# Kernel tuning notes

Hardware: AMD Instinct MI355X
Metric: run time of the kernel (lower is better)

## Reference

```python
import jax, jax.numpy as jnp
import numpy as np

EPS = 1e-8  # torch cosine_similarity clamps norms at 1e-8
TEMPERATURE = 0.05


def _normalize(x):
    n = jnp.linalg.norm(x, axis=-1, keepdims=True)
    return x / jnp.maximum(n, EPS)


def setup_inputs() -> dict:
    key = jax.random.key(0)
    k1, k2, k3 = jax.random.split(key, 3)
    N, D = 8192, 256
    return {
        "text_embeddings": jax.random.normal(k1, (N, D), dtype=jnp.float32),
        "text_pos_embeddings": jax.random.normal(k2, (N, D), dtype=jnp.float32),
        "text_neg_embeddings": jax.random.normal(k3, (N, D), dtype=jnp.float32),
    }


def _pair_loss(a, b):
    # PairInBatchNegCoSentLoss(a, b): cos-sim matrix, scale, diag-subtract, LSE
    sim = _normalize(a) @ _normalize(b).T / TEMPERATURE  # [N, N]
    diff = sim - jnp.diagonal(sim)[:, None]
    return jax.nn.logsumexp(diff, axis=1).mean()


def reference(text_embeddings, text_pos_embeddings, text_neg_embeddings):
    e = _normalize(text_embeddings)
    p = _normalize(text_pos_embeddings)
    n = _normalize(text_neg_embeddings)
    sim_pos = jnp.sum(e * p, axis=-1)          # [N]
    sim_neg = e @ n.T                          # [N, N]
    sim = jnp.concatenate([sim_pos[:, None], sim_neg], axis=1) / TEMPERATURE
    diff = sim - sim[:, 0:1]
    loss = jax.nn.logsumexp(diff, axis=1).mean()
    # add_swap_loss=True: pair loss with (pos, anchor) swapped
    loss = loss + _pair_loss(text_pos_embeddings, text_embeddings)
    return loss
```

## Files before the change

kernel.cpp:

```cpp
#include <hip/hip_runtime.h>
#include <stdint.h>

#define N 8192
#define D 256
#define INV_T 20.0f
#define LOG2E 1.44269504088896340736f
#define BM 128
#define BN 128
#define NXB 64

typedef __attribute__((ext_vector_type(16))) float f32x16;
typedef __attribute__((ext_vector_type(4))) int i32x4;
typedef __attribute__((ext_vector_type(8))) int i32x8;

typedef __attribute__((address_space(3))) uint32_t lds_u32;
typedef __attribute__((address_space(1))) const uint32_t gbl_u32;

static __device__ __forceinline__ float fast_exp2(float x) {
#if __has_builtin(__builtin_amdgcn_exp2f)
  return __builtin_amdgcn_exp2f(x);
#else
  float r;
  asm("v_exp_f32 %0, %1" : "=v"(r) : "v"(x));
  return r;
#endif
}

#define DPP_ADD(v, ctrl)                                                      \
  ((v) + __builtin_bit_cast(float, __builtin_amdgcn_update_dpp(               \
             0, __builtin_bit_cast(int, (v)), (ctrl), 0xf, 0xf, true)))

__global__ __launch_bounds__(256) void normalize_kernel(
    const float* __restrict__ e, const float* __restrict__ p, const float* __restrict__ n,
    uint32_t* __restrict__ eb, uint32_t* __restrict__ pb, uint32_t* __restrict__ nb,
    float* __restrict__ cbuf) {
  const int tid = threadIdx.x;
  const int wave = tid >> 6, lane = tid & 63;
  const int row = blockIdx.x * 4 + wave;

  const float4 ev = ((const float4*)(e + (size_t)row * D))[lane];
  const float4 pv = ((const float4*)(p + (size_t)row * D))[lane];
  const float4 nv = ((const float4*)(n + (size_t)row * D))[lane];

  float sse = ev.x*ev.x + ev.y*ev.y + ev.z*ev.z + ev.w*ev.w;
  float ssp = pv.x*pv.x + pv.y*pv.y + pv.z*pv.z + pv.w*pv.w;
  float ssn = nv.x*nv.x + nv.y*nv.y + nv.z*nv.z + nv.w*nv.w;
  float dep = ev.x*pv.x + ev.y*pv.y + ev.z*pv.z + ev.w*pv.w;
#pragma unroll
  for (int m = 1; m < 64; m <<= 1) {
    sse += __shfl_xor(sse, m);
    ssp += __shfl_xor(ssp, m);
    ssn += __shfl_xor(ssn, m);
    dep += __shfl_xor(dep, m);
  }
  const float se = 1.0f / fmaxf(sqrtf(sse), 1e-8f);
  const float sp = 1.0f / fmaxf(sqrtf(ssp), 1e-8f);
  const float sn = 1.0f / fmaxf(sqrtf(ssn), 1e-8f);

  int ue = __builtin_amdgcn_cvt_pk_fp8_f32(ev.x*se, ev.y*se, 0, false);
  ue     = __builtin_amdgcn_cvt_pk_fp8_f32(ev.z*se, ev.w*se, ue, true);
  int up = __builtin_amdgcn_cvt_pk_fp8_f32(pv.x*sp, pv.y*sp, 0, false);
  up     = __builtin_amdgcn_cvt_pk_fp8_f32(pv.z*sp, pv.w*sp, up, true);
  int un = __builtin_amdgcn_cvt_pk_fp8_f32(nv.x*sn, nv.y*sn, 0, false);
  un     = __builtin_amdgcn_cvt_pk_fp8_f32(nv.z*sn, nv.w*sn, un, true);
  eb[row * 64 + lane] = (uint32_t)ue;
  pb[row * 64 + lane] = (uint32_t)up;
  nb[row * 64 + lane] = (uint32_t)un;

  if (lane == 0) cbuf[row] = dep * se * sp * INV_T;
}

__global__ __launch_bounds__(256, 3) void simexp_kernel(
    const uint8_t* __restrict__ eb, const uint8_t* __restrict__ pb,
    const uint8_t* __restrict__ nb, const float* __restrict__ cbuf,
    float* __restrict__ part) {
  __shared__ uint8_t Bs[BN * D];
  __shared__ float cs[BM];

  const int z = blockIdx.z;
  const uint8_t* __restrict__ A = z ? pb : eb;
  const uint8_t* __restrict__ B = z ? eb : nb;

  const int tid = threadIdx.x;
  const int wave = tid >> 6, lane = tid & 63;
  const int lane31 = lane & 31, half = lane >> 5;
  const int rowTile = blockIdx.x * BM, colblk = blockIdx.y;
  const int colTile = colblk * BN;

#pragma unroll
  for (int i = 0; i < 8; ++i) {
    const int c = i * 256 + tid, r = c >> 4, sl = c & 15;
    const int gg = sl ^ (r & 15);
    __builtin_amdgcn_global_load_lds(
        (gbl_u32*)(B + (size_t)(colTile + r) * D + gg * 16),
        (lds_u32*)&Bs[c * 16], 16, 0, 0);
  }

  const int arow = rowTile + wave * 32 + lane31;
  const uint8_t* __restrict__ Arow = A + (size_t)arow * D + half * 32;
  i32x8 afr[4];
#pragma unroll
  for (int s = 0; s < 4; ++s) {
    const i32x4 lo = *(const i32x4*)(Arow + s * 64);
    const i32x4 hi = *(const i32x4*)(Arow + s * 64 + 16);
    afr[s] = (i32x8){lo[0], lo[1], lo[2], lo[3], hi[0], hi[1], hi[2], hi[3]};
  }

  if (tid < BM) cs[tid] = cbuf[rowTile + tid] * LOG2E;

  int bbase[4];
#pragma unroll
  for (int ni = 0; ni < 4; ++ni) {
    const int cl = ni * 32 + lane31;
    bbase[ni] = (cl << 8) ^ ((cl & 15) << 4) ^ (half << 5);
  }

  f32x16 acc[4];
#pragma unroll
  for (int ni = 0; ni < 4; ++ni)
#pragma unroll
    for (int r = 0; r < 16; ++r) acc[ni][r] = 0.0f;

  __syncthreads();

#pragma unroll
  for (int s = 0; s < 4; ++s) {
#pragma unroll
    for (int ni = 0; ni < 4; ++ni) {
      const int alo = bbase[ni] ^ (s << 6);
      const i32x4 blo = *(const i32x4*)&Bs[alo];
      const i32x4 bhi = *(const i32x4*)&Bs[alo ^ 16];
      const i32x8 b = (i32x8){blo[0], blo[1], blo[2], blo[3],
                              bhi[0], bhi[1], bhi[2], bhi[3]};
      acc[ni] = __builtin_amdgcn_mfma_scale_f32_32x32x64_f8f6f4(
          afr[s], b, acc[ni],
          0 , 0 ,
          0, 0x7F7F7F7F , 0, 0x7F7F7F7F );
    }
  }

  const float K2 = INV_T * LOG2E;
#pragma unroll
  for (int reg = 0; reg < 16; ++reg) {
    const int rlocal = (reg & 3) + 8 * (reg >> 2) + 4 * half;
    const int rowl = wave * 32 + rlocal;
    const float cv = cs[rowl];
    float v = fast_exp2(acc[0][reg] * K2 - cv) + fast_exp2(acc[1][reg] * K2 - cv) +
              fast_exp2(acc[2][reg] * K2 - cv) + fast_exp2(acc[3][reg] * K2 - cv);
    v = DPP_ADD(v, 0xB1);
    v = DPP_ADD(v, 0x4E);
    v = DPP_ADD(v, 0x141);
    v = DPP_ADD(v, 0x140);
    v += __builtin_bit_cast(float, __builtin_amdgcn_ds_swizzle(
             __builtin_bit_cast(int, v), 0x401F));
    if (lane31 == 0)
      part[((size_t)(z * NXB + colblk)) * N + rowTile + rowl] = v;
  }
}

__global__ __launch_bounds__(64) void reduce1_kernel(const float* __restrict__ part,
                                                     float* __restrict__ partials) {
  const int bid = blockIdx.x;
  const int z = bid >> 7;
  const int row = (bid & 127) * 64 + threadIdx.x;
  float s = 0.0f;
#pragma unroll 8
  for (int x = 0; x < NXB; ++x)
    s += part[((size_t)(z * NXB + x)) * N + row];
  float val = z ? logf(s) : log1pf(s);
#pragma unroll
  for (int m = 1; m < 64; m <<= 1) val += __shfl_xor(val, m);
  if (threadIdx.x == 0) partials[bid] = val;
}

__global__ __launch_bounds__(256) void reduce2_kernel(const float* __restrict__ partials,
                                                      float* __restrict__ out) {
  const int tid = threadIdx.x;
  float v = partials[tid];
#pragma unroll
  for (int m = 1; m < 64; m <<= 1) v += __shfl_xor(v, m);
  __shared__ float sm[4];
  if ((tid & 63) == 0) sm[tid >> 6] = v;
  __syncthreads();
  if (tid == 0) out[0] = (sm[0] + sm[1] + sm[2] + sm[3]) * (1.0f / (float)N);
}

extern "C" void kernel_launch(void* const* d_in, const int* in_sizes, int n_in,
                              void* d_out, int out_size, void* d_ws, size_t ws_size,
                              hipStream_t stream) {
  const float* e = (const float*)d_in[0];
  const float* p = (const float*)d_in[1];
  const float* n = (const float*)d_in[2];

  char* w = (char*)d_ws;
  uint8_t* eb = (uint8_t*)w;
  uint8_t* pb = eb + (size_t)N * D;
  uint8_t* nb = pb + (size_t)N * D;
  float* cbuf = (float*)(nb + (size_t)N * D);
  float* part = cbuf + N;
  float* partials = part + (size_t)2 * NXB * N;

  normalize_kernel<<<N / 4, 256, 0, stream>>>(e, p, n, (uint32_t*)eb, (uint32_t*)pb,
                                              (uint32_t*)nb, cbuf);
  simexp_kernel<<<dim3(N / BM, N / BN, 2), 256, 0, stream>>>(eb, pb, nb, cbuf, part);
  reduce1_kernel<<<256, 64, 0, stream>>>(part, partials);
  reduce2_kernel<<<1, 256, 0, stream>>>(partials, (float*)d_out);
}
```

Before: 127.5 us.

## Fuse final reductions via atomic counter, raise occupancy, prioritize MFMA waves

Merges the two reduction kernels into one by having the last block to finish (detected through an atomic counter reset in the normalize kernel) perform the final sum, which removes one kernel launch. It also raises simexp launch bounds from 3 to 4 waves-per-SIMD occupancy, wraps the MFMA loop in s_setprio to favor matrix-issuing waves, and forces the inline-asm v_exp_f32 path. The changes trade a threadfence plus atomic for launch overhead, and the higher occupancy may constrain registers.

New measurement: 137.0 us. +7.4%, slower.

```diff
diff --git a/kernel.cpp b/kernel.cpp
--- a/kernel.cpp
+++ b/kernel.cpp
@@ -17,13 +17,9 @@
 typedef __attribute__((address_space(1))) const uint32_t gbl_u32;
 
 static __device__ __forceinline__ float fast_exp2(float x) {
-#if __has_builtin(__builtin_amdgcn_exp2f)
-  return __builtin_amdgcn_exp2f(x);
-#else
   float r;
   asm("v_exp_f32 %0, %1" : "=v"(r) : "v"(x));
   return r;
-#endif
 }
 
 #define DPP_ADD(v, ctrl)                                                      \
@@ -33,10 +29,12 @@
 __global__ __launch_bounds__(256) void normalize_kernel(
     const float* __restrict__ e, const float* __restrict__ p, const float* __restrict__ n,
     uint32_t* __restrict__ eb, uint32_t* __restrict__ pb, uint32_t* __restrict__ nb,
-    float* __restrict__ cbuf) {
+    float* __restrict__ cbuf, uint32_t* __restrict__ counter) {
   const int tid = threadIdx.x;
   const int wave = tid >> 6, lane = tid & 63;
   const int row = blockIdx.x * 4 + wave;
+
+  if (blockIdx.x == 0 && tid == 0) *counter = 0u;
 
   const float4 ev = ((const float4*)(e + (size_t)row * D))[lane];
   const float4 pv = ((const float4*)(p + (size_t)row * D))[lane];
@@ -70,7 +68,7 @@
   if (lane == 0) cbuf[row] = dep * se * sp * INV_T;
 }
 
-__global__ __launch_bounds__(256, 3) void simexp_kernel(
+__global__ __launch_bounds__(256, 4) void simexp_kernel(
     const uint8_t* __restrict__ eb, const uint8_t* __restrict__ pb,
     const uint8_t* __restrict__ nb, const float* __restrict__ cbuf,
     float* __restrict__ part) {
@@ -123,6 +121,7 @@
 
   __syncthreads();
 
+  __builtin_amdgcn_s_setprio(1);
 #pragma unroll
   for (int s = 0; s < 4; ++s) {
 #pragma unroll
@@ -138,6 +137,7 @@
           0, 0x7F7F7F7F , 0, 0x7F7F7F7F );
     }
   }
+  __builtin_amdgcn_s_setprio(0);
 
   const float K2 = INV_T * LOG2E;
 #pragma unroll
@@ -158,8 +158,10 @@
   }
 }
 
-__global__ __launch_bounds__(64) void reduce1_kernel(const float* __restrict__ part,
-                                                     float* __restrict__ partials) {
+__global__ __launch_bounds__(64) void reduce_kernel(const float* __restrict__ part,
+                                                    float* __restrict__ partials,
+                                                    uint32_t* __restrict__ counter,
+                                                    float* __restrict__ out) {
   const int bid = blockIdx.x;
   const int z = bid >> 7;
   const int row = (bid & 127) * 64 + threadIdx.x;
@@ -171,18 +173,20 @@
 #pragma unroll
   for (int m = 1; m < 64; m <<= 1) val += __shfl_xor(val, m);
   if (threadIdx.x == 0) partials[bid] = val;
-}
-
-__global__ __launch_bounds__(256) void reduce2_kernel(const float* __restrict__ partials,
-                                                      float* __restrict__ out) {
-  const int tid = threadIdx.x;
-  float v = partials[tid];
-#pragma unroll
-  for (int m = 1; m < 64; m <<= 1) v += __shfl_xor(v, m);
-  __shared__ float sm[4];
-  if ((tid & 63) == 0) sm[tid >> 6] = v;
+
+  __threadfence();
+  __shared__ bool lastb;
+  if (threadIdx.x == 0)
+    lastb = (atomicAdd(counter, 1u) == 255u);
   __syncthreads();
-  if (tid == 0) out[0] = (sm[0] + sm[1] + sm[2] + sm[3]) * (1.0f / (float)N);
+  if (lastb) {
+    __threadfence();
+    const int t = threadIdx.x;
+    float v = partials[t] + partials[t + 64] + partials[t + 128] + partials[t + 192];
+#pragma unroll
+    for (int m = 1; m < 64; m <<= 1) v += __shfl_xor(v, m);
+    if (t == 0) out[0] = v * (1.0f / (float)N);
+  }
 }
 
 extern "C" void kernel_launch(void* const* d_in, const int* in_sizes, int n_in,
@@ -199,10 +203,10 @@
   float* cbuf = (float*)(nb + (size_t)N * D);
   float* part = cbuf + N;
   float* partials = part + (size_t)2 * NXB * N;
+  uint32_t* counter = (uint32_t*)(partials + 256);
 
   normalize_kernel<<<N / 4, 256, 0, stream>>>(e, p, n, (uint32_t*)eb, (uint32_t*)pb,
-                                              (uint32_t*)nb, cbuf);
+                                              (uint32_t*)nb, cbuf, counter);
   simexp_kernel<<<dim3(N / BM, N / BN, 2), 256, 0, stream>>>(eb, pb, nb, cbuf, part);
-  reduce1_kernel<<<256, 64, 0, stream>>>(part, partials);
-  reduce2_kernel<<<1, 256, 0, stream>>>(partials, (float*)d_out);
-}
+  reduce_kernel<<<256, 64, 0, stream>>>(part, partials, counter, (float*)d_out);
+}
```
